# Kernel tuning notes

Hardware: AMD Instinct MI355X
Metric: run time of the kernel (lower is better)

## Reference

```python
import math
import jax, jax.numpy as jnp
import numpy as np

B, N, CS, CZ, CH, H, PQ, PV = 1, 4096, 512, 128, 64, 16, 4, 8
BQ, BK = 32, 128
NB = N // BQ
CZ4 = CZ // 4
INF = 100000.0
EPS = 1e-8


def quat_to_rot(q):
    w, x, y, z = q[..., 0], q[..., 1], q[..., 2], q[..., 3]
    return jnp.stack([
        jnp.stack([1 - 2 * (y * y + z * z), 2 * (x * y - w * z), 2 * (x * z + w * y)], -1),
        jnp.stack([2 * (x * y + w * z), 1 - 2 * (x * x + z * z), 2 * (y * z - w * x)], -1),
        jnp.stack([2 * (x * z - w * y), 2 * (y * z + w * x), 1 - 2 * (x * x + y * y)], -1),
    ], -2)


def setup_inputs() -> dict:
    key = jax.random.key(0)
    ks = jax.random.split(key, 16)
    s = jax.random.normal(ks[0], (B, N, CS), jnp.float32)
    z = jax.random.normal(ks[1], (B, NB, BQ, BK, CZ), jnp.float32)
    trans = jax.random.normal(ks[2], (B, N, 3), jnp.float32) * 10.0
    quat = jax.random.normal(ks[3], (B, N, 4), jnp.float32)
    quat = quat / jnp.linalg.norm(quat, axis=-1, keepdims=True)
    rots = quat_to_rot(quat)
    s_mask = jnp.ones((B, N), jnp.float32)
    pad = (BK - BQ) // 2  # key window centered on each query block
    key_idx = (jnp.arange(NB)[:, None] * BQ - pad + jnp.arange(BK)[None, :]).astype(jnp.int32)

    def w(k, shp):
        return jax.random.normal(k, shp, jnp.float32) * (1.0 / math.sqrt(shp[0]))

    return {
        's': s, 'z': z, 'trans': trans, 'rots': rots, 's_mask': s_mask, 'key_idx': key_idx,
        'Wq': w(ks[4], (CS, H * CH)), 'Wk': w(ks[5], (CS, H * CH)), 'Wv': w(ks[6], (CS, H * CH)),
        'Wqp': w(ks[7], (CS, H * PQ * 3)), 'Wkvp': w(ks[8], (CS, H * (PQ + PV) * 3)),
        'Wb': w(ks[9], (CZ, H)), 'Wdz': w(ks[10], (CZ, CZ4)),
        'head_weights': jnp.full((H,), float(np.log(np.e - 1.0)), jnp.float32),  # softplus^-1(1)
        'Wout': w(ks[11], (H * (CZ4 + CH + PV * 4), CS)),
        'g_s': jnp.ones((CS,), jnp.float32), 'b_s': jnp.zeros((CS,), jnp.float32),
        'g_z': jnp.ones((CZ,), jnp.float32), 'b_z': jnp.zeros((CZ,), jnp.float32),
    }


def _ln(x, g, b):
    m = jnp.mean(x, -1, keepdims=True)
    v = jnp.mean((x - m) ** 2, -1, keepdims=True)
    return (x - m) * jax.lax.rsqrt(v + 1e-5) * g + b


def _ipa(s, z, trans, rots, s_mask, key_idx, Wq, Wk, Wv, Wqp, Wkvp, Wb, Wdz,
         head_weights, Wout, g_s, b_s, g_z, b_z):
    s_n = _ln(s, g_s, b_s)
    z_n = _ln(z, g_z, b_z)

    valid = (key_idx >= 0) & (key_idx < N)            # [NB, BK]
    idx = jnp.clip(key_idx, 0, N - 1)
    vf = valid.astype(s.dtype)[None]                  # [1, NB, BK]

    def gk(x):  # gather key window: [B,N,...] -> [B,NB,BK,...]
        return x[:, idx]

    sq = s_n.reshape(B, NB, BQ, CS)
    sk = gk(s_n) * vf[..., None]                      # zero-pad out-of-range keys

    tq = trans.reshape(B, NB, BQ, 3)
    rq = rots.reshape(B, NB, BQ, 3, 3)
    tk = gk(trans) * vf[..., None]
    rk = jnp.where(valid[None, :, :, None, None], gk(rots), jnp.eye(3, dtype=rots.dtype))

    q = (sq @ Wq).reshape(B, NB, BQ, H, CH)
    k = (sk @ Wk).reshape(B, NB, BK, H, CH)
    v = (sk @ Wv).reshape(B, NB, BK, H, CH)

    q_pts = (sq @ Wqp).reshape(B, NB, BQ, H * PQ, 3)
    q_pts = jnp.einsum('bnqij,bnqpj->bnqpi', rq, q_pts) + tq[:, :, :, None, :]
    q_pts = q_pts.reshape(B, NB, BQ, H, PQ, 3)

    kv_pts = (sk @ Wkvp).reshape(B, NB, BK, H * (PQ + PV), 3)
    kv_pts = jnp.einsum('bnkij,bnkpj->bnkpi', rk, kv_pts) + tk[:, :, :, None, :]
    kv_pts = kv_pts.reshape(B, NB, BK, H, PQ + PV, 3)
    k_pts, v_pts = kv_pts[..., :PQ, :], kv_pts[..., PQ:, :]

    bias = jnp.einsum('bnqkc,ch->bnqkh', z_n, Wb)
    a = jnp.einsum('bnqhc,bnkhc->bnqkh', q, k) * math.sqrt(1.0 / (3 * CH))
    a = a + math.sqrt(1.0 / 3) * bias

    disp = q_pts[:, :, :, None] - k_pts[:, :, None]   # [B,NB,BQ,BK,H,PQ,3]
    pt_att = jnp.sum(disp ** 2, -1)                   # [B,NB,BQ,BK,H,PQ]
    hw = jax.nn.softplus(head_weights) * math.sqrt(1.0 / (3 * (PQ * 9.0 / 2)))
    pt_att = -0.5 * jnp.sum(pt_att * hw[:, None], -1)  # [B,NB,BQ,BK,H]

    qm = s_mask.reshape(B, NB, BQ)
    km = gk(s_mask) * vf
    amask = INF * (qm[:, :, :, None] * km[:, :, None, :] - 1.0)

    a = a + pt_att + amask[..., None]
    a = jax.nn.softmax(jnp.swapaxes(a, -1, -2), axis=-1)  # [B,NB,BQ,H,BK]

    o = jnp.einsum('bnqhk,bnkhc->bnqhc', a, v).reshape(B, NB, BQ, H * CH)

    o_pt = jnp.einsum('bnqhk,bnkhpc->bnqhpc', a, v_pts)
    o_pt = jnp.einsum('bnqji,bnqhpj->bnqhpi', rq, o_pt - tq[:, :, :, None, None, :])
    o_pt_norm = jnp.sqrt(jnp.sum(o_pt ** 2, -1) + EPS).reshape(B, NB, BQ, H * PV)
    o_pt = o_pt.reshape(B, NB, BQ, H * PV * 3)

    pair_z = z_n @ Wdz                                # [B,NB,BQ,BK,CZ4]
    o_pair = jnp.einsum('bnqhk,bnqkc->bnqhc', a, pair_z).reshape(B, NB, BQ, H * CZ4)

    out = jnp.concatenate([o, o_pt, o_pt_norm, o_pair], -1) @ Wout
    return out.reshape(B, N, CS)


def reference(s, z, trans, rots, s_mask, key_idx, Wq, Wk, Wv, Wqp, Wkvp, Wb, Wdz,
              head_weights, Wout, g_s, b_s, g_z, b_z):
    return _ipa(s, z, trans, rots, s_mask, key_idx, Wq, Wk, Wv, Wqp, Wkvp, Wb, Wdz,
                head_weights, Wout, g_s, b_s, g_z, b_z)
```

## Files before the change

### kernel.cpp

```cpp
#include <hip/hip_runtime.h>
#include <math.h>

#define D_N 4096
#define PBW 3072
#define PPW 768
#define OFFK 1024
#define OFFV 2048
#define CATW 2048

typedef __bf16 bf16_t;
typedef __bf16 bf16x8 __attribute__((ext_vector_type(8)));
typedef __bf16 bf16x4 __attribute__((ext_vector_type(4)));
typedef float f32x4 __attribute__((ext_vector_type(4)));

__device__ __forceinline__ void gld16(const void* g, void* l) {
    __builtin_amdgcn_global_load_lds((const __attribute__((address_space(1))) unsigned int*)g,
                                     (__attribute__((address_space(3))) unsigned int*)l, 16, 0, 0);
}

__global__ __launch_bounds__(256) void k_prep(
    const float* __restrict__ Wq, const float* __restrict__ Wk, const float* __restrict__ Wv,
    const float* __restrict__ Wqp, const float* __restrict__ Wkvp, const float* __restrict__ Wout,
    const float* __restrict__ Wb, const float* __restrict__ Wdz,
    const float* __restrict__ gz, const float* __restrict__ bz,
    const float* __restrict__ s, const float* __restrict__ g_s, const float* __restrict__ b_s,
    bf16_t* __restrict__ wcatT, bf16_t* __restrict__ WoutT,
    bf16_t* __restrict__ WzT, float* __restrict__ Kv, bf16_t* __restrict__ s_nb)
{
    __shared__ float T[64][65];
    const int bx = blockIdx.x;
    const int tid = threadIdx.x;
    if (bx < 736) {
        const float* src; int ld, coff, r0;
        bf16_t* dst; int Rdst;
        if (bx < 480) {
            int c0 = (bx % 60) * 64;
            r0 = (bx / 60) * 64;
            if (c0 < 1024)      { src = Wq;   ld = 1024; coff = c0; }
            else if (c0 < 2048) { src = Wk;   ld = 1024; coff = c0 - 1024; }
            else if (c0 < 3072) { src = Wv;   ld = 1024; coff = c0 - 2048; }
            else if (c0 < 3264) { src = Wqp;  ld = 192;  coff = c0 - 3072; }
            else                { src = Wkvp; ld = 576;  coff = c0 - 3264; }
            dst = wcatT + (size_t)c0 * 512; Rdst = 512;
        } else {
            int b = bx - 480;
            int c0 = (b & 7) * 64;
            r0 = (b >> 3) * 64;
            src = Wout; ld = 512; coff = c0;
            dst = WoutT + (size_t)c0 * 2048; Rdst = 2048;
        }
        {
            int rr = tid >> 2, cb = (tid & 3) * 16;
            const float* p = src + (size_t)(r0 + rr) * ld + coff + cb;
            #pragma unroll
            for (int i = 0; i < 4; ++i)
                *(float4*)&T[rr][cb + i * 4] = *(const float4*)(p + i * 4);
        }
        __syncthreads();
        {
            int cc = tid >> 2, rb = (tid & 3) * 16;
            bf16_t* o = dst + (size_t)cc * Rdst + r0 + rb;
            bf16x8 o0, o1;
            #pragma unroll
            for (int j = 0; j < 8; ++j) o0[j] = (bf16_t)T[rb + j][cc];
            #pragma unroll
            for (int j = 0; j < 8; ++j) o1[j] = (bf16_t)T[rb + 8 + j][cc];
            *(bf16x8*)(o) = o0;
            *(bf16x8*)(o + 8) = o1;
        }
    } else if (bx == 736) {
        for (int i = tid; i < 6144; i += 256) {
            int j = i >> 7, c = i & 127;
            float w = (j < 16) ? Wb[c * 16 + j] : Wdz[c * 32 + (j - 16)];
            WzT[i] = (bf16_t)(gz[c] * w);
        }
        if (tid < 48) {
            int j = tid;
            float acc = 0.f;
            for (int c = 0; c < 128; ++c) {
                float w = (j < 16) ? Wb[c * 16 + j] : Wdz[c * 32 + (j - 16)];
                acc += bz[c] * w;
            }
            Kv[j] = acc;
        }
    } else {
        int row = (bx - 737) * 4 + (tid >> 6);
        int lane = tid & 63;
        const float4* p = (const float4*)(s + (size_t)row * 512);
        float4 v0 = p[lane];
        float4 v1 = p[lane + 64];
        float sum = v0.x + v0.y + v0.z + v0.w + v1.x + v1.y + v1.z + v1.w;
        float sq  = v0.x*v0.x + v0.y*v0.y + v0.z*v0.z + v0.w*v0.w
                  + v1.x*v1.x + v1.y*v1.y + v1.z*v1.z + v1.w*v1.w;
        #pragma unroll
        for (int off = 1; off < 64; off <<= 1) {
            sum += __shfl_xor(sum, off);
            sq  += __shfl_xor(sq, off);
        }
        float m = sum * (1.0f / 512.0f);
        float var = sq * (1.0f / 512.0f) - m * m;
        float rs = rsqrtf(var + 1e-5f);
        int c = lane * 4;
        int c2 = 256 + lane * 4;
        bf16x4 r0, r1;
        r0[0] = (bf16_t)((v0.x - m) * rs * g_s[c+0] + b_s[c+0]);
        r0[1] = (bf16_t)((v0.y - m) * rs * g_s[c+1] + b_s[c+1]);
        r0[2] = (bf16_t)((v0.z - m) * rs * g_s[c+2] + b_s[c+2]);
        r0[3] = (bf16_t)((v0.w - m) * rs * g_s[c+3] + b_s[c+3]);
        r1[0] = (bf16_t)((v1.x - m) * rs * g_s[c2+0] + b_s[c2+0]);
        r1[1] = (bf16_t)((v1.y - m) * rs * g_s[c2+1] + b_s[c2+1]);
        r1[2] = (bf16_t)((v1.z - m) * rs * g_s[c2+2] + b_s[c2+2]);
        r1[3] = (bf16_t)((v1.w - m) * rs * g_s[c2+3] + b_s[c2+3]);
        *(bf16x4*)(s_nb + (size_t)row * 512 + c)  = r0;
        *(bf16x4*)(s_nb + (size_t)row * 512 + c2) = r1;
    }
}

__global__ __launch_bounds__(256) void gemm_proj(const bf16_t* __restrict__ A, const bf16_t* __restrict__ BT,
    bf16_t* __restrict__ projb, float* __restrict__ projp)
{
    __shared__ bf16_t Asl[128][32];
    __shared__ bf16_t Bsl[128][32];
    const int tid = threadIdx.x, lane = tid & 63, w = tid >> 6;
    const int row0 = blockIdx.y * 128, col0 = blockIdx.x * 128;
    const int wr = (w >> 1) * 64, wc = (w & 1) * 64;
    const int K = 512;
    const int sr = lane >> 2, k8 = (lane & 3) * 8;
    const bf16_t* Ab = A + (size_t)(row0 + w * 32 + sr) * K + k8;
    const bf16_t* Bb = BT + (size_t)(col0 + w * 32 + sr) * K + k8;
    f32x4 acc[4][4];
    #pragma unroll
    for (int m = 0; m < 4; ++m)
        #pragma unroll
        for (int n = 0; n < 4; ++n) acc[m][n] = (f32x4){0.f,0.f,0.f,0.f};
    for (int k0 = 0; k0 < K; k0 += 32) {
        __syncthreads();
        gld16(Ab + k0,          &Asl[w * 32][0]);
        gld16(Ab + k0 + 16 * K, &Asl[w * 32 + 16][0]);
        gld16(Bb + k0,          &Bsl[w * 32][0]);
        gld16(Bb + k0 + 16 * K, &Bsl[w * 32 + 16][0]);
        __syncthreads();
        bf16x8 af[4], bfr[4];
        #pragma unroll
        for (int m = 0; m < 4; ++m) af[m]  = *(const bf16x8*)&Asl[wr + m*16 + (lane & 15)][(lane >> 4) * 8];
        #pragma unroll
        for (int n = 0; n < 4; ++n) bfr[n] = *(const bf16x8*)&Bsl[wc + n*16 + (lane & 15)][(lane >> 4) * 8];
        #pragma unroll
        for (int m = 0; m < 4; ++m)
            #pragma unroll
            for (int n = 0; n < 4; ++n)
                acc[m][n] = __builtin_amdgcn_mfma_f32_16x16x32_bf16(af[m], bfr[n], acc[m][n], 0, 0, 0);
    }
    if (col0 < 3072) {
        #pragma unroll
        for (int m = 0; m < 4; ++m)
            #pragma unroll
            for (int n = 0; n < 4; ++n)
                #pragma unroll
                for (int i = 0; i < 4; ++i)
                    projb[(size_t)(row0 + wr + m*16 + (lane >> 4)*4 + i) * PBW + col0 + wc + n*16 + (lane & 15)]
                        = (bf16_t)acc[m][n][i];
    } else {
        #pragma unroll
        for (int m = 0; m < 4; ++m)
            #pragma unroll
            for (int n = 0; n < 4; ++n)
                #pragma unroll
                for (int i = 0; i < 4; ++i)
                    projp[(size_t)(row0 + wr + m*16 + (lane >> 4)*4 + i) * PPW + col0 - 3072 + wc + n*16 + (lane & 15)]
                        = acc[m][n][i];
    }
}

__global__ __launch_bounds__(256) void gemm_out(const bf16_t* __restrict__ A, const bf16_t* __restrict__ BT,
    float* __restrict__ C)
{
    __shared__ bf16_t Asl[128][32];
    __shared__ bf16_t Bsl[128][32];
    const int tid = threadIdx.x, lane = tid & 63, w = tid >> 6;
    const int row0 = blockIdx.y * 128, col0 = blockIdx.x * 128;
    const int wr = (w >> 1) * 64, wc = (w & 1) * 64;
    const int K = 2048;
    const int sr = lane >> 2, k8 = (lane & 3) * 8;
    const bf16_t* Ab = A + (size_t)(row0 + w * 32 + sr) * K + k8;
    const bf16_t* Bb = BT + (size_t)(col0 + w * 32 + sr) * K + k8;
    f32x4 acc[4][4];
    #pragma unroll
    for (int m = 0; m < 4; ++m)
        #pragma unroll
        for (int n = 0; n < 4; ++n) acc[m][n] = (f32x4){0.f,0.f,0.f,0.f};
    for (int k0 = 0; k0 < K; k0 += 32) {
        __syncthreads();
        gld16(Ab + k0,          &Asl[w * 32][0]);
        gld16(Ab + k0 + 16 * K, &Asl[w * 32 + 16][0]);
        gld16(Bb + k0,          &Bsl[w * 32][0]);
        gld16(Bb + k0 + 16 * K, &Bsl[w * 32 + 16][0]);
        __syncthreads();
        bf16x8 af[4], bfr[4];
        #pragma unroll
        for (int m = 0; m < 4; ++m) af[m]  = *(const bf16x8*)&Asl[wr + m*16 + (lane & 15)][(lane >> 4) * 8];
        #pragma unroll
        for (int n = 0; n < 4; ++n) bfr[n] = *(const bf16x8*)&Bsl[wc + n*16 + (lane & 15)][(lane >> 4) * 8];
        #pragma unroll
        for (int m = 0; m < 4; ++m)
            #pragma unroll
            for (int n = 0; n < 4; ++n)
                acc[m][n] = __builtin_amdgcn_mfma_f32_16x16x32_bf16(af[m], bfr[n], acc[m][n], 0, 0, 0);
    }
    #pragma unroll
    for (int m = 0; m < 4; ++m)
        #pragma unroll
        for (int n = 0; n < 4; ++n)
            #pragma unroll
            for (int i = 0; i < 4; ++i)
                C[(size_t)(row0 + wr + m*16 + (lane >> 4)*4 + i) * 512 + col0 + wc + n*16 + (lane & 15)] = acc[m][n][i];
}

__global__ __launch_bounds__(256) void k_zrot(const float* __restrict__ z,
    const bf16_t* __restrict__ WzT, const float* __restrict__ Kv,
    float* __restrict__ biasT, bf16_t* __restrict__ pzT,
    float* __restrict__ projp, const float* __restrict__ rots, const float* __restrict__ trans)
{
    __shared__ __align__(16) float zbuf[2][64][128];
    const int tid = threadIdx.x, lane = tid & 63, w = tid >> 6;
    if (blockIdx.x >= 2048) {
        int row = (blockIdx.x - 2048) * 4 + (tid >> 6);
        const float* R = rots + (size_t)row * 9;
        const float* t = trans + (size_t)row * 3;
        float R0=R[0],R1=R[1],R2=R[2],R3=R[3],R4=R[4],R5=R[5],R6=R[6],R7=R[7],R8=R[8];
        float t0=t[0],t1=t[1],t2=t[2];
        float* base = projp + (size_t)row * PPW + lane * 12;
        float4 a = *(const float4*)(base);
        float4 b = *(const float4*)(base + 4);
        float4 c = *(const float4*)(base + 8);
        float x0=a.x,y0=a.y,z0=a.z, x1=a.w,y1=b.x,z1=b.y, x2=b.z,y2=b.w,z2=c.x, x3=c.y,y3=c.z,z3=c.w;
        a.x = R0*x0+R1*y0+R2*z0+t0; a.y = R3*x0+R4*y0+R5*z0+t1; a.z = R6*x0+R7*y0+R8*z0+t2;
        a.w = R0*x1+R1*y1+R2*z1+t0; b.x = R3*x1+R4*y1+R5*z1+t1; b.y = R6*x1+R7*y1+R8*z1+t2;
        b.z = R0*x2+R1*y2+R2*z2+t0; b.w = R3*x2+R4*y2+R5*z2+t1; c.x = R6*x2+R7*y2+R8*z2+t2;
        c.y = R0*x3+R1*y3+R2*z3+t0; c.z = R3*x3+R4*y3+R5*z3+t1; c.w = R6*x3+R7*y3+R8*z3+t2;
        *(float4*)(base) = a;
        *(float4*)(base + 4) = b;
        *(float4*)(base + 8) = c;
        return;
    }
    const int r16 = lane & 15, kg = lane >> 4;
    bf16x8 bfz[3][4];
    #pragma unroll
    for (int nt = 0; nt < 3; ++nt)
        #pragma unroll
        for (int kc = 0; kc < 4; ++kc)
            bfz[nt][kc] = *(const bf16x8*)(WzT + (size_t)(nt * 16 + r16) * 128 + kc * 32 + kg * 8);
    float K0 = Kv[r16], K1 = Kv[16 + r16], K2 = Kv[32 + r16];
    asm volatile("s_waitcnt vmcnt(0)" ::: "memory");

    const int gid = blockIdx.x * 4 + w;
    const char* zb = (const char*)z + (size_t)gid * 64 * 512;
    char* lb0 = (char*)&zbuf[0][w * 16][0];
    char* lb1 = (char*)&zbuf[1][w * 16][0];

#define STAGE(i, lb) { \
    const char* gp_ = zb + (size_t)(i) * 8192 + lane * 16; \
    _Pragma("unroll") \
    for (int c_ = 0; c_ < 8; ++c_) gld16(gp_ + c_ * 1024, (lb) + c_ * 1024); }

#define PROCESS(i, b) { \
    const float* rp = &zbuf[b][w * 16 + r16][kg * 8]; \
    float4 za[4], zc[4]; \
    float sum = 0.f, sq = 0.f; \
    _Pragma("unroll") \
    for (int kc = 0; kc < 4; ++kc) { \
        float4 a_ = *(const float4*)(rp + kc * 32); \
        float4 b_ = *(const float4*)(rp + kc * 32 + 4); \
        za[kc] = a_; zc[kc] = b_; \
        sum += a_.x + a_.y + a_.z + a_.w + b_.x + b_.y + b_.z + b_.w; \
        sq  += a_.x*a_.x + a_.y*a_.y + a_.z*a_.z + a_.w*a_.w + b_.x*b_.x + b_.y*b_.y + b_.z*b_.z + b_.w*b_.w; \
    } \
    sum += __shfl_xor(sum, 16); sq += __shfl_xor(sq, 16); \
    sum += __shfl_xor(sum, 32); sq += __shfl_xor(sq, 32); \
    float m_ = sum * (1.0f / 128.0f); \
    float rs_ = rsqrtf(sq * (1.0f / 128.0f) - m_ * m_ + 1e-5f); \
    bf16x8 af[4]; \
    _Pragma("unroll") \
    for (int kc = 0; kc < 4; ++kc) { \
        af[kc][0] = (bf16_t)((za[kc].x - m_) * rs_); \
        af[kc][1] = (bf16_t)((za[kc].y - m_) * rs_); \
        af[kc][2] = (bf16_t)((za[kc].z - m_) * rs_); \
        af[kc][3] = (bf16_t)((za[kc].w - m_) * rs_); \
        af[kc][4] = (bf16_t)((zc[kc].x - m_) * rs_); \
        af[kc][5] = (bf16_t)((zc[kc].y - m_) * rs_); \
        af[kc][6] = (bf16_t)((zc[kc].z - m_) * rs_); \
        af[kc][7] = (bf16_t)((zc[kc].w - m_) * rs_); \
    } \
    f32x4 acc0 = (f32x4){0.f,0.f,0.f,0.f}; \
    f32x4 acc1 = (f32x4){0.f,0.f,0.f,0.f}; \
    f32x4 acc2 = (f32x4){0.f,0.f,0.f,0.f}; \
    _Pragma("unroll") \
    for (int kc = 0; kc < 4; ++kc) { \
        acc0 = __builtin_amdgcn_mfma_f32_16x16x32_bf16(af[kc], bfz[0][kc], acc0, 0, 0, 0); \
        acc1 = __builtin_amdgcn_mfma_f32_16x16x32_bf16(af[kc], bfz[1][kc], acc1, 0, 0, 0); \
        acc2 = __builtin_amdgcn_mfma_f32_16x16x32_bf16(af[kc], bfz[2][kc], acc2, 0, 0, 0); \
    } \
    const int t_ = gid * 4 + (i); \
    const int rowq_ = t_ >> 3; \
    const int k0_ = ((t_ & 7) << 4) + kg * 4; \
    float4 bw = {acc0[0] + K0, acc0[1] + K0, acc0[2] + K0, acc0[3] + K0}; \
    *(float4*)&biasT[((size_t)rowq_ * 16 + r16) * 128 + k0_] = bw; \
    bf16x4 p1, p2; \
    _Pragma("unroll") \
    for (int i2 = 0; i2 < 4; ++i2) { p1[i2] = (bf16_t)(acc1[i2] + K1); p2[i2] = (bf16_t)(acc2[i2] + K2); } \
    *(bf16x4*)&pzT[((size_t)rowq_ * 32 + r16) * 128 + k0_] = p1; \
    *(bf16x4*)&pzT[((size_t)rowq_ * 32 + 16 + r16) * 128 + k0_] = p2; }

    STAGE(0, lb0);
    STAGE(1, lb1);
    asm volatile("s_waitcnt vmcnt(8)" ::: "memory");
    PROCESS(0, 0);
    STAGE(2, lb0);
    asm volatile("s_waitcnt vmcnt(11)" ::: "memory");
    PROCESS(1, 1);
    STAGE(3, lb1);
    asm volatile("s_waitcnt vmcnt(11)" ::: "memory");
    PROCESS(2, 0);
    asm volatile("s_waitcnt vmcnt(3)" ::: "memory");
    PROCESS(3, 1);
#undef STAGE
#undef PROCESS
}

__global__ __launch_bounds__(256) void k_attn3(
    const bf16_t* __restrict__ projb, const float* __restrict__ projp,
    const float* __restrict__ biasT, const float* __restrict__ rots,
    const float* __restrict__ trans, const float* __restrict__ smask,
    const int* __restrict__ kidx, const float* __restrict__ hwraw,
    bf16_t* __restrict__ catb, bf16_t* __restrict__ Pbf)
{
    __shared__ __align__(16) char uni[26112];
    __shared__ float att[32][132];
    __shared__ float kp_s[128][12];
    __shared__ float qp_s[32][12];
    __shared__ bf16_t Ps[32][136];
    __shared__ float optmp[32][33];
    __shared__ float km_s[128];
    __shared__ float qm_s[32];
    __shared__ int   rows_s[128];

    bf16_t (*Qs)[72]  = (bf16_t(*)[72])uni;
    bf16_t (*Ks)[72]  = (bf16_t(*)[72])(uni + 32 * 72 * 2);
    bf16_t (*Vt)[136] = (bf16_t(*)[136])uni;

    const int wgid = blockIdx.x;
    const int swz = (wgid & 7) * 256 + (wgid >> 3);
    const int h = swz >> 7;
    const int nblk = swz & 127;
    const int tid = threadIdx.x;
    const int lane = tid & 63;
    const int w = tid >> 6;
    const int rowq0 = nblk * 32;
    const float hw = log1pf(__expf(hwraw[h])) * 0.13608276348795434f;

    if (tid < 128) {
        int ki = kidx[nblk * 128 + tid];
        int valid = (ki >= 0 && ki < D_N);
        int rr = ki < 0 ? 0 : (ki > D_N - 1 ? D_N - 1 : ki);
        rows_s[tid] = rr;
        km_s[tid] = valid ? smask[rr] : 0.0f;
    } else if (tid < 160) {
        qm_s[tid - 128] = smask[rowq0 + tid - 128];
    }
    __syncthreads();
    {
        int q = tid >> 3, cg = (tid & 7) * 8;
        *(bf16x8*)&Qs[q][cg] = *(const bf16x8*)(projb + (size_t)(rowq0 + q) * PBW + h * 64 + cg);
    }
    if (tid < 128) {
        int q = tid >> 2, dg = (tid & 3) * 3;
        const float* p = projp + (size_t)(rowq0 + q) * PPW + h * 12 + dg;
        qp_s[q][dg + 0] = p[0]; qp_s[q][dg + 1] = p[1]; qp_s[q][dg + 2] = p[2];
    }
    {
        int krow = tid >> 1, cg = (tid & 1) * 32;
        const bf16_t* p = projb + (size_t)rows_s[krow] * PBW + OFFK + h * 64 + cg;
        #pragma unroll
        for (int u = 0; u < 4; ++u)
            *(bf16x8*)&Ks[krow][cg + u * 8] = *(const bf16x8*)(p + u * 8);
        const float* pk = projp + (size_t)rows_s[krow] * PPW + 192 + h * 36 + (tid & 1) * 6;
        int dg = (tid & 1) * 6;
        #pragma unroll
        for (int u = 0; u < 6; ++u) kp_s[krow][dg + u] = pk[u];
    }
    __syncthreads();
    {
        #pragma unroll
        for (int j = 0; j < 4; ++j) {
            int T = w * 4 + j;
            int m = T & 1, n = T >> 1;
            f32x4 acc = (f32x4){0.f,0.f,0.f,0.f};
            #pragma unroll
            for (int kc = 0; kc < 2; ++kc) {
                bf16x8 a = *(const bf16x8*)&Qs[m*16 + (lane & 15)][kc*32 + (lane >> 4) * 8];
                bf16x8 b = *(const bf16x8*)&Ks[n*16 + (lane & 15)][kc*32 + (lane >> 4) * 8];
                acc = __builtin_amdgcn_mfma_f32_16x16x32_bf16(a, b, acc, 0, 0, 0);
            }
            #pragma unroll
            for (int i = 0; i < 4; ++i)
                att[m*16 + (lane >> 4)*4 + i][n*16 + (lane & 15)] = acc[i];
        }
    }
    __syncthreads();
    {
        int krow = tid >> 1, cg = (tid & 1) * 32;
        const bf16_t* p = projb + (size_t)rows_s[krow] * PBW + OFFV + h * 64 + cg;
        #pragma unroll
        for (int u4 = 0; u4 < 4; ++u4) {
            bf16x8 v = *(const bf16x8*)(p + u4 * 8);
            #pragma unroll
            for (int j = 0; j < 8; ++j) Vt[cg + u4 * 8 + j][krow] = v[j];
        }
        const float* pv = projp + (size_t)rows_s[krow] * PPW + 192 + h * 36 + 12 + (tid & 1) * 12;
        #pragma unroll
        for (int u = 0; u < 3; ++u) {
            float4 v = *(const float4*)(pv + u * 4);
            int rb = 64 + (tid & 1) * 12 + u * 4;
            Vt[rb + 0][krow] = (bf16_t)v.x;
            Vt[rb + 1][krow] = (bf16_t)v.y;
            Vt[rb + 2][krow] = (bf16_t)v.z;
            Vt[rb + 3][krow] = (bf16_t)v.w;
        }
        {
            int r = 88 + (tid >> 5), c = (tid & 31) * 4;
            bf16x4 zz; zz[0]=(bf16_t)0.f; zz[1]=(bf16_t)0.f; zz[2]=(bf16_t)0.f; zz[3]=(bf16_t)0.f;
            *(bf16x4*)&Vt[r][c] = zz;
        }
        int q = tid >> 3, kg = tid & 7;
        float qp[12];
        #pragma unroll
        for (int e = 0; e < 12; ++e) qp[e] = qp_s[q][e];
        float qm = qm_s[q];
        const float* bT = biasT + ((size_t)(rowq0 + q) * 16 + h) * 128;
        #pragma unroll
        for (int j2 = 0; j2 < 16; ++j2) {
            int k = kg + j2 * 8;
            float4 k0 = *(const float4*)&kp_s[k][0];
            float4 k1 = *(const float4*)&kp_s[k][4];
            float4 k2 = *(const float4*)&kp_s[k][8];
            float d0 = qp[0]-k0.x, d1 = qp[1]-k0.y, d2_ = qp[2]-k0.z, d3 = qp[3]-k0.w;
            float d4 = qp[4]-k1.x, d5 = qp[5]-k1.y, d6 = qp[6]-k1.z, d7 = qp[7]-k1.w;
            float d8 = qp[8]-k2.x, d9 = qp[9]-k2.y, d10 = qp[10]-k2.z, d11 = qp[11]-k2.w;
            float dd = d0*d0+d1*d1+d2_*d2_+d3*d3+d4*d4+d5*d5+d6*d6+d7*d7+d8*d8+d9*d9+d10*d10+d11*d11;
            float val = att[q][k] * 0.07216878364870323f
                      + 0.5773502691896258f * bT[k]
                      + 100000.0f * (qm * km_s[k] - 1.0f)
                      - 0.5f * hw * dd;
            att[q][k] = val;
        }
    }
    __syncthreads();
    {
        int q = tid >> 3, kg = tid & 7;
        float l[16];
        #pragma unroll
        for (int j2 = 0; j2 < 16; ++j2) l[j2] = att[q][kg + j2 * 8];
        float mx = l[0];
        #pragma unroll
        for (int j2 = 1; j2 < 16; ++j2) mx = fmaxf(mx, l[j2]);
        mx = fmaxf(mx, __shfl_xor(mx, 1));
        mx = fmaxf(mx, __shfl_xor(mx, 2));
        mx = fmaxf(mx, __shfl_xor(mx, 4));
        float se = 0.f;
        #pragma unroll
        for (int j2 = 0; j2 < 16; ++j2) { l[j2] = __expf(l[j2] - mx); se += l[j2]; }
        se += __shfl_xor(se, 1);
        se += __shfl_xor(se, 2);
        se += __shfl_xor(se, 4);
        float inv = 1.0f / se;
        bf16_t* pg = Pbf + ((size_t)(rowq0 + q) * 16 + h) * 128;
        #pragma unroll
        for (int j2 = 0; j2 < 16; ++j2) {
            bf16_t pb = (bf16_t)(l[j2] * inv);
            Ps[q][kg + j2 * 8] = pb;
            pg[kg + j2 * 8] = pb;
        }
    }
    __syncthreads();
    {
        #pragma unroll
        for (int j = 0; j < 3; ++j) {
            int T = w * 3 + j;
            int m = T & 1, n = T >> 1;
            f32x4 acc = (f32x4){0.f,0.f,0.f,0.f};
            #pragma unroll
            for (int kc = 0; kc < 4; ++kc) {
                bf16x8 a = *(const bf16x8*)&Ps[m*16 + (lane & 15)][kc*32 + (lane >> 4) * 8];
                bf16x8 b = *(const bf16x8*)&Vt[n*16 + (lane & 15)][kc*32 + (lane >> 4) * 8];
                acc = __builtin_amdgcn_mfma_f32_16x16x32_bf16(a, b, acc, 0, 0, 0);
            }
            int rowb = m * 16 + (lane >> 4) * 4;
            int col = lane & 15;
            if (n < 4) {
                #pragma unroll
                for (int i = 0; i < 4; ++i)
                    catb[(size_t)(rowq0 + rowb + i) * CATW + h * 64 + n * 16 + col] = (bf16_t)acc[i];
            } else {
                #pragma unroll
                for (int i = 0; i < 4; ++i)
                    optmp[rowb + i][(n - 4) * 16 + col] = acc[i];
            }
        }
    }
    __syncthreads();
    {
        int q = tid >> 3, pp = tid & 7;
        float sx = optmp[q][pp * 3 + 0];
        float sy = optmp[q][pp * 3 + 1];
        float sz = optmp[q][pp * 3 + 2];
        const float* R = rots + (size_t)(rowq0 + q) * 9;
        const float* t = trans + (size_t)(rowq0 + q) * 3;
        float x = sx - t[0], y = sy - t[1], z2 = sz - t[2];
        float ox = R[0] * x + R[3] * y + R[6] * z2;
        float oy = R[1] * x + R[4] * y + R[7] * z2;
        float oz = R[2] * x + R[5] * y + R[8] * z2;
        bf16_t* cp = catb + (size_t)(rowq0 + q) * CATW;
        cp[1024 + h * 24 + pp * 3 + 0] = (bf16_t)ox;
        cp[1024 + h * 24 + pp * 3 + 1] = (bf16_t)oy;
        cp[1024 + h * 24 + pp * 3 + 2] = (bf16_t)oz;
        cp[1408 + h * 8 + pp] = (bf16_t)sqrtf(ox * ox + oy * oy + oz * oz + 1e-8f);
    }
}

__global__ __launch_bounds__(256) void k_opair(const bf16_t* __restrict__ Pbf,
    const bf16_t* __restrict__ pzT, bf16_t* __restrict__ catb)
{
    int tid = threadIdx.x, lane = tid & 63, w = tid >> 6;
    size_t rowq = (size_t)blockIdx.x * 4 + w;
    const bf16_t* Pp = Pbf + rowq * 2048;
    const bf16_t* zp = pzT + rowq * 4096;
    bf16x8 pa[4];
    #pragma unroll
    for (int kc = 0; kc < 4; ++kc)
        pa[kc] = *(const bf16x8*)(Pp + (size_t)(lane & 15) * 128 + kc * 32 + (lane >> 4) * 8);
    #pragma unroll
    for (int ct = 0; ct < 2; ++ct) {
        f32x4 acc = (f32x4){0.f,0.f,0.f,0.f};
        #pragma unroll
        for (int kc = 0; kc < 4; ++kc) {
            bf16x8 b = *(const bf16x8*)(zp + (size_t)(ct * 16 + (lane & 15)) * 128 + kc * 32 + (lane >> 4) * 8);
            acc = __builtin_amdgcn_mfma_f32_16x16x32_bf16(pa[kc], b, acc, 0, 0, 0);
        }
        #pragma unroll
        for (int i = 0; i < 4; ++i) {
            int hh = (lane >> 4) * 4 + i;
            catb[rowq * CATW + 1536 + hh * 32 + ct * 16 + (lane & 15)] = (bf16_t)acc[i];
        }
    }
}

extern "C" void kernel_launch(void* const* d_in, const int* in_sizes, int n_in,
                              void* d_out, int out_size, void* d_ws, size_t ws_size,
                              hipStream_t stream)
{
    (void)in_sizes; (void)n_in; (void)out_size;
    const float* s     = (const float*)d_in[0];
    const float* z     = (const float*)d_in[1];
    const float* trans = (const float*)d_in[2];
    const float* rots  = (const float*)d_in[3];
    const float* smask = (const float*)d_in[4];
    const int*   kidx  = (const int*)d_in[5];
    const float* Wq    = (const float*)d_in[6];
    const float* Wk    = (const float*)d_in[7];
    const float* Wv    = (const float*)d_in[8];
    const float* Wqp   = (const float*)d_in[9];
    const float* Wkvp  = (const float*)d_in[10];
    const float* Wb    = (const float*)d_in[11];
    const float* Wdz   = (const float*)d_in[12];
    const float* hw    = (const float*)d_in[13];
    const float* Wout  = (const float*)d_in[14];
    const float* g_s   = (const float*)d_in[15];
    const float* b_s   = (const float*)d_in[16];
    const float* g_z   = (const float*)d_in[17];
    const float* b_z   = (const float*)d_in[18];

    char* ws = (char*)d_ws;
    bf16_t* projb = (bf16_t*)(ws);
    float*  projp = (float*)(ws + 25165824);
    float*  biasT = (float*)(ws + 37748736);
    bf16_t* wcatT = (bf16_t*)(ws + 71303168);
    bf16_t* s_nb  = (bf16_t*)(ws + 75235328);
    bf16_t* pzT   = (bf16_t*)(ws + 79429632);
    bf16_t* Pbf   = (bf16_t*)(ws + 112984064);
    bf16_t* catb  = (bf16_t*)(ws + 129761280);
    bf16_t* WoutT = (bf16_t*)(ws + 146538496);
    bf16_t* WzT   = (bf16_t*)(ws + 148635648);
    float*  Kv    = (float*)(ws + 148647936);
    if (ws_size < (size_t)148648128) return;
    float* out = (float*)d_out;

    k_prep<<<1761, 256, 0, stream>>>(Wq, Wk, Wv, Wqp, Wkvp, Wout, Wb, Wdz, g_z, b_z,
                                     s, g_s, b_s, wcatT, WoutT, WzT, Kv, s_nb);
    gemm_proj<<<dim3(30, 32), 256, 0, stream>>>(s_nb, wcatT, projb, projp);
    k_zrot<<<3072, 256, 0, stream>>>(z, WzT, Kv, biasT, pzT, projp, rots, trans);
    k_attn3<<<2048, 256, 0, stream>>>(projb, projp, biasT, rots, trans, smask, kidx, hw, catb, Pbf);
    k_opair<<<1024, 256, 0, stream>>>(Pbf, pzT, catb);
    gemm_out<<<dim3(4, 32), 256, 0, stream>>>(catb, WoutT, out);
}
```

Baseline: 230.8 us.

## Fuse point rotation into attention loads, retile output GEMM, tighten z pipeline waits

Moves the rigid-frame transform of query, key and value points out of a separate block range in the z-bias kernel and into k_attn3. There each block rotates the points it loads into shared memory, which removes a read-modify-write pass over projp. Key points are re-rotated for every head, trading recomputation for less global traffic. The output GEMM moves to 64-row tiles, doubling the block count to 256 so more CUs are busy. The z-bias kernel gets scheduling barriers and adjusted vmcnt waits around its staged loads.

```diff
diff --git a/kernel.cpp b/kernel.cpp
--- a/kernel.cpp
+++ b/kernel.cpp
@@ -172,77 +172,12 @@
     }
 }
 
-__global__ __launch_bounds__(256) void gemm_out(const bf16_t* __restrict__ A, const bf16_t* __restrict__ BT,
-    float* __restrict__ C)
-{
-    __shared__ bf16_t Asl[128][32];
-    __shared__ bf16_t Bsl[128][32];
-    const int tid = threadIdx.x, lane = tid & 63, w = tid >> 6;
-    const int row0 = blockIdx.y * 128, col0 = blockIdx.x * 128;
-    const int wr = (w >> 1) * 64, wc = (w & 1) * 64;
-    const int K = 2048;
-    const int sr = lane >> 2, k8 = (lane & 3) * 8;
-    const bf16_t* Ab = A + (size_t)(row0 + w * 32 + sr) * K + k8;
-    const bf16_t* Bb = BT + (size_t)(col0 + w * 32 + sr) * K + k8;
-    f32x4 acc[4][4];
-    #pragma unroll
-    for (int m = 0; m < 4; ++m)
-        #pragma unroll
-        for (int n = 0; n < 4; ++n) acc[m][n] = (f32x4){0.f,0.f,0.f,0.f};
-    for (int k0 = 0; k0 < K; k0 += 32) {
-        __syncthreads();
-        gld16(Ab + k0,          &Asl[w * 32][0]);
-        gld16(Ab + k0 + 16 * K, &Asl[w * 32 + 16][0]);
-        gld16(Bb + k0,          &Bsl[w * 32][0]);
-        gld16(Bb + k0 + 16 * K, &Bsl[w * 32 + 16][0]);
-        __syncthreads();
-        bf16x8 af[4], bfr[4];
-        #pragma unroll
-        for (int m = 0; m < 4; ++m) af[m]  = *(const bf16x8*)&Asl[wr + m*16 + (lane & 15)][(lane >> 4) * 8];
-        #pragma unroll
-        for (int n = 0; n < 4; ++n) bfr[n] = *(const bf16x8*)&Bsl[wc + n*16 + (lane & 15)][(lane >> 4) * 8];
-        #pragma unroll
-        for (int m = 0; m < 4; ++m)
-            #pragma unroll
-            for (int n = 0; n < 4; ++n)
-                acc[m][n] = __builtin_amdgcn_mfma_f32_16x16x32_bf16(af[m], bfr[n], acc[m][n], 0, 0, 0);
-    }
-    #pragma unroll
-    for (int m = 0; m < 4; ++m)
-        #pragma unroll
-        for (int n = 0; n < 4; ++n)
-            #pragma unroll
-            for (int i = 0; i < 4; ++i)
-                C[(size_t)(row0 + wr + m*16 + (lane >> 4)*4 + i) * 512 + col0 + wc + n*16 + (lane & 15)] = acc[m][n][i];
-}
-
-__global__ __launch_bounds__(256) void k_zrot(const float* __restrict__ z,
+__global__ __launch_bounds__(256) void k_zbias4(const float* __restrict__ z,
     const bf16_t* __restrict__ WzT, const float* __restrict__ Kv,
-    float* __restrict__ biasT, bf16_t* __restrict__ pzT,
-    float* __restrict__ projp, const float* __restrict__ rots, const float* __restrict__ trans)
+    float* __restrict__ biasT, bf16_t* __restrict__ pzT)
 {
     __shared__ __align__(16) float zbuf[2][64][128];
     const int tid = threadIdx.x, lane = tid & 63, w = tid >> 6;
-    if (blockIdx.x >= 2048) {
-        int row = (blockIdx.x - 2048) * 4 + (tid >> 6);
-        const float* R = rots + (size_t)row * 9;
-        const float* t = trans + (size_t)row * 3;
-        float R0=R[0],R1=R[1],R2=R[2],R3=R[3],R4=R[4],R5=R[5],R6=R[6],R7=R[7],R8=R[8];
-        float t0=t[0],t1=t[1],t2=t[2];
-        float* base = projp + (size_t)row * PPW + lane * 12;
-        float4 a = *(const float4*)(base);
-        float4 b = *(const float4*)(base + 4);
-        float4 c = *(const float4*)(base + 8);
-        float x0=a.x,y0=a.y,z0=a.z, x1=a.w,y1=b.x,z1=b.y, x2=b.z,y2=b.w,z2=c.x, x3=c.y,y3=c.z,z3=c.w;
-        a.x = R0*x0+R1*y0+R2*z0+t0; a.y = R3*x0+R4*y0+R5*z0+t1; a.z = R6*x0+R7*y0+R8*z0+t2;
-        a.w = R0*x1+R1*y1+R2*z1+t0; b.x = R3*x1+R4*y1+R5*z1+t1; b.y = R6*x1+R7*y1+R8*z1+t2;
-        b.z = R0*x2+R1*y2+R2*z2+t0; b.w = R3*x2+R4*y2+R5*z2+t1; c.x = R6*x2+R7*y2+R8*z2+t2;
-        c.y = R0*x3+R1*y3+R2*z3+t0; c.z = R3*x3+R4*y3+R5*z3+t1; c.w = R6*x3+R7*y3+R8*z3+t2;
-        *(float4*)(base) = a;
-        *(float4*)(base + 4) = b;
-        *(float4*)(base + 8) = c;
-        return;
-    }
     const int r16 = lane & 15, kg = lane >> 4;
     bf16x8 bfz[3][4];
     #pragma unroll
@@ -252,6 +187,7 @@
             bfz[nt][kc] = *(const bf16x8*)(WzT + (size_t)(nt * 16 + r16) * 128 + kc * 32 + kg * 8);
     float K0 = Kv[r16], K1 = Kv[16 + r16], K2 = Kv[32 + r16];
     asm volatile("s_waitcnt vmcnt(0)" ::: "memory");
+    __builtin_amdgcn_sched_barrier(0);
 
     const int gid = blockIdx.x * 4 + w;
     const char* zb = (const char*)z + (size_t)gid * 64 * 512;
@@ -314,14 +250,18 @@
     STAGE(0, lb0);
     STAGE(1, lb1);
     asm volatile("s_waitcnt vmcnt(8)" ::: "memory");
+    __builtin_amdgcn_sched_barrier(0);
     PROCESS(0, 0);
     STAGE(2, lb0);
-    asm volatile("s_waitcnt vmcnt(11)" ::: "memory");
+    asm volatile("s_waitcnt vmcnt(8)" ::: "memory");
+    __builtin_amdgcn_sched_barrier(0);
     PROCESS(1, 1);
     STAGE(3, lb1);
-    asm volatile("s_waitcnt vmcnt(11)" ::: "memory");
+    asm volatile("s_waitcnt vmcnt(8)" ::: "memory");
+    __builtin_amdgcn_sched_barrier(0);
     PROCESS(2, 0);
-    asm volatile("s_waitcnt vmcnt(3)" ::: "memory");
+    asm volatile("s_waitcnt vmcnt(0)" ::: "memory");
+    __builtin_amdgcn_sched_barrier(0);
     PROCESS(3, 1);
 #undef STAGE
 #undef PROCESS
@@ -372,21 +312,45 @@
         int q = tid >> 3, cg = (tid & 7) * 8;
         *(bf16x8*)&Qs[q][cg] = *(const bf16x8*)(projb + (size_t)(rowq0 + q) * PBW + h * 64 + cg);
     }
+    float Rk[9], tk0 = 0.f, tk1 = 0.f, tk2 = 0.f;
     if (tid < 128) {
-        int q = tid >> 2, dg = (tid & 3) * 3;
-        const float* p = projp + (size_t)(rowq0 + q) * PPW + h * 12 + dg;
-        qp_s[q][dg + 0] = p[0]; qp_s[q][dg + 1] = p[1]; qp_s[q][dg + 2] = p[2];
-    }
-    {
-        int krow = tid >> 1, cg = (tid & 1) * 32;
-        const bf16_t* p = projb + (size_t)rows_s[krow] * PBW + OFFK + h * 64 + cg;
-        #pragma unroll
-        for (int u = 0; u < 4; ++u)
-            *(bf16x8*)&Ks[krow][cg + u * 8] = *(const bf16x8*)(p + u * 8);
-        const float* pk = projp + (size_t)rows_s[krow] * PPW + 192 + h * 36 + (tid & 1) * 6;
-        int dg = (tid & 1) * 6;
-        #pragma unroll
-        for (int u = 0; u < 6; ++u) kp_s[krow][dg + u] = pk[u];
+        int rr = rows_s[tid];
+        const float* Rp = rots + (size_t)rr * 9;
+        const float* tp = trans + (size_t)rr * 3;
+        #pragma unroll
+        for (int e = 0; e < 9; ++e) Rk[e] = Rp[e];
+        tk0 = tp[0]; tk1 = tp[1]; tk2 = tp[2];
+        const float* kp = projp + (size_t)rr * PPW + 192 + h * 36;
+        float4 p0 = *(const float4*)kp;
+        float4 p1 = *(const float4*)(kp + 4);
+        float4 p2 = *(const float4*)(kp + 8);
+        float xs[4] = {p0.x, p0.w, p1.z, p2.y};
+        float ys[4] = {p0.y, p1.x, p1.w, p2.z};
+        float zs[4] = {p0.z, p1.y, p2.x, p2.w};
+        #pragma unroll
+        for (int p = 0; p < 4; ++p) {
+            kp_s[tid][p*3+0] = Rk[0]*xs[p] + Rk[1]*ys[p] + Rk[2]*zs[p] + tk0;
+            kp_s[tid][p*3+1] = Rk[3]*xs[p] + Rk[4]*ys[p] + Rk[5]*zs[p] + tk1;
+            kp_s[tid][p*3+2] = Rk[6]*xs[p] + Rk[7]*ys[p] + Rk[8]*zs[p] + tk2;
+        }
+    } else {
+        int j = tid - 128;
+        {
+            int q = j >> 2, p = j & 3;
+            const float* Rp = rots + (size_t)(rowq0 + q) * 9;
+            const float* tp = trans + (size_t)(rowq0 + q) * 3;
+            const float* qp = projp + (size_t)(rowq0 + q) * PPW + h * 12 + p * 3;
+            float x = qp[0], y = qp[1], zc = qp[2];
+            qp_s[q][p*3+0] = Rp[0]*x + Rp[1]*y + Rp[2]*zc + tp[0];
+            qp_s[q][p*3+1] = Rp[3]*x + Rp[4]*y + Rp[5]*zc + tp[1];
+            qp_s[q][p*3+2] = Rp[6]*x + Rp[7]*y + Rp[8]*zc + tp[2];
+        }
+        {
+            const bf16_t* pK = projb + (size_t)rows_s[j] * PBW + OFFK + h * 64;
+            #pragma unroll
+            for (int u = 0; u < 8; ++u)
+                *(bf16x8*)&Ks[j][u * 8] = *(const bf16x8*)(pK + u * 8);
+        }
     }
     __syncthreads();
     {
@@ -407,30 +371,38 @@
         }
     }
     __syncthreads();
+    if (tid < 128) {
+        const float* vp = projp + (size_t)rows_s[tid] * PPW + 192 + h * 36 + 12;
+        float4 a0 = *(const float4*)(vp);
+        float4 a1 = *(const float4*)(vp + 4);
+        float4 a2 = *(const float4*)(vp + 8);
+        float4 a3 = *(const float4*)(vp + 12);
+        float4 a4 = *(const float4*)(vp + 16);
+        float4 a5 = *(const float4*)(vp + 20);
+        float xs[8] = {a0.x, a0.w, a1.z, a2.y, a3.x, a3.w, a4.z, a5.y};
+        float ys[8] = {a0.y, a1.x, a1.w, a2.z, a3.y, a4.x, a4.w, a5.z};
+        float zs[8] = {a0.z, a1.y, a2.x, a2.w, a3.z, a4.y, a5.x, a5.w};
+        #pragma unroll
+        for (int p = 0; p < 8; ++p) {
+            Vt[64 + p*3 + 0][tid] = (bf16_t)(Rk[0]*xs[p] + Rk[1]*ys[p] + Rk[2]*zs[p] + tk0);
+            Vt[64 + p*3 + 1][tid] = (bf16_t)(Rk[3]*xs[p] + Rk[4]*ys[p] + Rk[5]*zs[p] + tk1);
+            Vt[64 + p*3 + 2][tid] = (bf16_t)(Rk[6]*xs[p] + Rk[7]*ys[p] + Rk[8]*zs[p] + tk2);
+        }
+        {
+            bf16x8 zz = {};
+            *(bf16x8*)&Vt[88 + (tid & 7)][(tid >> 3) * 8] = zz;
+        }
+    } else {
+        int krow = tid - 128;
+        const bf16_t* p = projb + (size_t)rows_s[krow] * PBW + OFFV + h * 64;
+        #pragma unroll
+        for (int u4 = 0; u4 < 8; ++u4) {
+            bf16x8 v = *(const bf16x8*)(p + u4 * 8);
+            #pragma unroll
+            for (int jj = 0; jj < 8; ++jj) Vt[u4 * 8 + jj][krow] = v[jj];
+        }
+    }
     {
-        int krow = tid >> 1, cg = (tid & 1) * 32;
-        const bf16_t* p = projb + (size_t)rows_s[krow] * PBW + OFFV + h * 64 + cg;
-        #pragma unroll
-        for (int u4 = 0; u4 < 4; ++u4) {
-            bf16x8 v = *(const bf16x8*)(p + u4 * 8);
-            #pragma unroll
-            for (int j = 0; j < 8; ++j) Vt[cg + u4 * 8 + j][krow] = v[j];
-        }
-        const float* pv = projp + (size_t)rows_s[krow] * PPW + 192 + h * 36 + 12 + (tid & 1) * 12;
-        #pragma unroll
-        for (int u = 0; u < 3; ++u) {
-            float4 v = *(const float4*)(pv + u * 4);
-            int rb = 64 + (tid & 1) * 12 + u * 4;
-            Vt[rb + 0][krow] = (bf16_t)v.x;
-            Vt[rb + 1][krow] = (bf16_t)v.y;
-            Vt[rb + 2][krow] = (bf16_t)v.z;
-            Vt[rb + 3][krow] = (bf16_t)v.w;
-        }
-        {
-            int r = 88 + (tid >> 5), c = (tid & 31) * 4;
-            bf16x4 zz; zz[0]=(bf16_t)0.f; zz[1]=(bf16_t)0.f; zz[2]=(bf16_t)0.f; zz[3]=(bf16_t)0.f;
-            *(bf16x4*)&Vt[r][c] = zz;
-        }
         int q = tid >> 3, kg = tid & 7;
         float qp[12];
         #pragma unroll
@@ -552,6 +524,49 @@
             catb[rowq * CATW + 1536 + hh * 32 + ct * 16 + (lane & 15)] = (bf16_t)acc[i];
         }
     }
+}
+
+__global__ __launch_bounds__(256) void gemm_out(const bf16_t* __restrict__ A, const bf16_t* __restrict__ BT,
+    float* __restrict__ C)
+{
+    __shared__ bf16_t Asl[64][32];
+    __shared__ bf16_t Bsl[128][32];
+    const int tid = threadIdx.x, lane = tid & 63, w = tid >> 6;
+    const int row0 = blockIdx.y * 64, col0 = blockIdx.x * 128;
+    const int wr = (w >> 1) * 32, wc = (w & 1) * 64;
+    const int K = 2048;
+    const int sr = lane >> 2, k8 = (lane & 3) * 8;
+    const bf16_t* Ab = A + (size_t)(row0 + w * 16 + sr) * K + k8;
+    const bf16_t* Bb = BT + (size_t)(col0 + w * 32 + sr) * K + k8;
+    f32x4 acc[2][4];
+    #pragma unroll
+    for (int m = 0; m < 2; ++m)
+        #pragma unroll
+        for (int n = 0; n < 4; ++n) acc[m][n] = (f32x4){0.f,0.f,0.f,0.f};
+    for (int k0 = 0; k0 < K; k0 += 32) {
+        __syncthreads();
+        gld16(Ab + k0,          &Asl[w * 16][0]);
+        gld16(Bb + k0,          &Bsl[w * 32][0]);
+        gld16(Bb + k0 + 16 * K, &Bsl[w * 32 + 16][0]);
+        __syncthreads();
+        bf16x8 af[2], bfr[4];
+        #pragma unroll
+        for (int m = 0; m < 2; ++m) af[m]  = *(const bf16x8*)&Asl[wr + m*16 + (lane & 15)][(lane >> 4) * 8];
+        #pragma unroll
+        for (int n = 0; n < 4; ++n) bfr[n] = *(const bf16x8*)&Bsl[wc + n*16 + (lane & 15)][(lane >> 4) * 8];
+        #pragma unroll
+        for (int m = 0; m < 2; ++m)
+            #pragma unroll
+            for (int n = 0; n < 4; ++n)
+                acc[m][n] = __builtin_amdgcn_mfma_f32_16x16x32_bf16(af[m], bfr[n], acc[m][n], 0, 0, 0);
+    }
+    #pragma unroll
+    for (int m = 0; m < 2; ++m)
+        #pragma unroll
+        for (int n = 0; n < 4; ++n)
+            #pragma unroll
+            for (int i = 0; i < 4; ++i)
+                C[(size_t)(row0 + wr + m*16 + (lane >> 4)*4 + i) * 512 + col0 + wc + n*16 + (lane & 15)] = acc[m][n][i];
 }
 
 extern "C" void kernel_launch(void* const* d_in, const int* in_sizes, int n_in,
@@ -597,8 +612,8 @@
     k_prep<<<1761, 256, 0, stream>>>(Wq, Wk, Wv, Wqp, Wkvp, Wout, Wb, Wdz, g_z, b_z,
                                      s, g_s, b_s, wcatT, WoutT, WzT, Kv, s_nb);
     gemm_proj<<<dim3(30, 32), 256, 0, stream>>>(s_nb, wcatT, projb, projp);
-    k_zrot<<<3072, 256, 0, stream>>>(z, WzT, Kv, biasT, pzT, projp, rots, trans);
+    k_zbias4<<<2048, 256, 0, stream>>>(z, WzT, Kv, biasT, pzT);
     k_attn3<<<2048, 256, 0, stream>>>(projb, projp, biasT, rots, trans, smask, kidx, hw, catb, Pbf);
     k_opair<<<1024, 256, 0, stream>>>(Pbf, pzT, catb);
-    gemm_out<<<dim3(4, 32), 256, 0, stream>>>(catb, WoutT, out);
-}
+    gemm_out<<<dim3(4, 64), 256, 0, stream>>>(catb, WoutT, out);
+}
```

Measured after the change: 221.6 us. 4.0% less time.
